# Performance work log

Measured on AMD Instinct MI355X. Metric: run time of the kernel, lower is better.

Reference implementation:

```python
import jax, jax.numpy as jnp
import numpy as np
from jax import lax

C = 256  # in_channels == out_channels
DN = ('NCHW', 'OIHW', 'NCHW')


def _haar_kernels(Cc, dtype):
    # Faithfully reproduce the torch buffer construction, INCLUDING its layout:
    # filters has shape (4*C, 1, 2, 2) with filters[f*C + c] = base[f]; the grouped
    # conv (groups=C) then applies filters[oc] (= base[oc // C]) to input channel oc // 4.
    lo = np.array([0.5, 0.5], np.float32)
    hi = np.array([0.5, -0.5], np.float32)
    # torch: dec_a.unsqueeze(0)*dec_b.unsqueeze(1) -> [i,j] = a[j]*b[i] = outer(b, a)
    dec_base = np.stack([np.outer(lo, lo), np.outer(hi, lo), np.outer(lo, hi), np.outer(hi, hi)], 0)
    dec_k = dec_base[np.arange(4 * Cc) // Cc][:, None]  # (4C, 1, 2, 2)
    rlo = np.array([1.0, 1.0], np.float32)
    rhi = np.array([1.0, -1.0], np.float32)
    rec_base = np.stack([np.outer(rlo, rlo), np.outer(rhi, rlo), np.outer(rlo, rhi), np.outer(rhi, rhi)], 0) / 2.0
    # conv_transpose2d(stride=2, groups=C) weight (4C, 1, 2, 2) with w[f*C + c] = rec_base[f].
    # Equivalent regular grouped conv (feature_group_count=C) kernel (C, 4, 2, 2):
    # K[g, f] = flip2(w[4g + f, 0]), applied with lhs_dilation=2, padding=1.
    w = rec_base[np.arange(4 * Cc) // Cc]
    rec_k = w.reshape(Cc, 4, 2, 2)[:, :, ::-1, ::-1].copy()
    return jnp.asarray(dec_k, dtype), jnp.asarray(rec_k, dtype)


def _dw(x, w, b=None):
    # depthwise 3x3 conv, padding=1
    y = lax.conv_general_dilated(x, w, (1, 1), [(1, 1), (1, 1)],
                                 feature_group_count=x.shape[1], dimension_numbers=DN)
    return y if b is None else y + b[None, :, None, None]


def setup_inputs() -> dict:
    key = jax.random.key(0)
    ks = jax.random.split(key, 12)
    p = lambda k, s: jax.random.normal(k, s, jnp.float32) * 0.1
    return {
        'x': jax.random.normal(ks[0], (4, C, 224, 224), jnp.float32),
        'base_w': p(ks[1], (C, 1, 3, 3)),
        'base_b': p(ks[2], (C,)),
        'base_scale': jnp.ones((1, C, 1, 1), jnp.float32),
        'wavelet_scale': jnp.full((1, C, 1, 1), 0.1, jnp.float32),
        'w_ll': p(ks[3], (C, 1, 3, 3)),
        'w_lh0': p(ks[4], (C, 1, 3, 3)),
        'w_hl0': p(ks[5], (C, 1, 3, 3)),
        'w_hh0': p(ks[6], (C, 1, 3, 3)),
        'w_lh1': p(ks[7], (C, 1, 3, 3)),
        'w_hl1': p(ks[8], (C, 1, 3, 3)),
        'w_hh1': p(ks[9], (C, 1, 3, 3)),
    }


def reference(x, base_w, base_b, base_scale, wavelet_scale, w_ll,
              w_lh0, w_hl0, w_hh0, w_lh1, w_hl1, w_hh1):
    B, Cc, H, W = x.shape
    dec_k, rec_k = _haar_kernels(Cc, x.dtype)

    def decompose(z):
        y = lax.conv_general_dilated(z, dec_k, (2, 2), 'VALID',
                                     feature_group_count=Cc, dimension_numbers=DN)
        y = y.reshape(B, Cc, 4, y.shape[-2], y.shape[-1])
        return y[:, :, 0], y[:, :, 1], y[:, :, 2], y[:, :, 3]  # ll, lh, hl, hh

    def reconstruct(ll, lh, hl, hh):
        comb = jnp.stack([ll, lh, hl, hh], 2).reshape(B, Cc * 4, ll.shape[-2], ll.shape[-1])
        return lax.conv_general_dilated(comb, rec_k, (1, 1), [(1, 1), (1, 1)],
                                        lhs_dilation=(2, 2), feature_group_count=Cc,
                                        dimension_numbers=DN)

    divisor = 4  # 2 ** depth
    pad_h, pad_w = (-H) % divisor, (-W) % divisor
    xp = jnp.pad(x, ((0, 0), (0, 0), (0, pad_h), (0, pad_w)), mode='reflect') if (pad_h or pad_w) else x

    # recursive DWT (depth=2)
    ll0, lh0, hl0, hh0 = decompose(xp)
    ll1, lh1, hl1, hh1 = decompose(ll0)

    # per-subband depthwise convs, then recursive IDWT
    x_wt = _dw(ll1, w_ll)  # only the deepest level's LL conv is used
    x_wt = reconstruct(x_wt, _dw(lh1, w_lh1), _dw(hl1, w_hl1), _dw(hh1, w_hh1))
    x_wt = reconstruct(x_wt, _dw(lh0, w_lh0), _dw(hl0, w_hl0), _dw(hh0, w_hh0))
    x_wt = x_wt[:, :, :H, :W] * wavelet_scale

    x_base = _dw(x, base_w, base_b) * base_scale
    return x_base + x_wt
```

## Files before the change

kernel.cpp:

```cpp
#include <hip/hip_runtime.h>


#define HH 224
#define WW 224
#define CC 256
#define BB 4
#define XS_S 68
#define T0_S 36

__global__ __launch_bounds__(256) void wtconv_fused(
    const float* __restrict__ x,
    const float* __restrict__ base_w,
    const float* __restrict__ base_b,
    const float* __restrict__ base_scale,
    const float* __restrict__ wavelet_scale,
    const float* __restrict__ w_ll,
    const float* __restrict__ w_lh0,
    const float* __restrict__ w_hl0,
    const float* __restrict__ w_hh0,
    const float* __restrict__ w_lh1,
    const float* __restrict__ w_hl1,
    const float* __restrict__ w_hh1,
    float* __restrict__ out)
{
    __shared__ float xs[64][XS_S];
    __shared__ float t0s[32][T0_S];
    __shared__ float t1s[16][18];
    __shared__ float a1s[14][14];
    __shared__ float a0s[28][28];

    const int tid  = threadIdx.x;
    const int bid  = blockIdx.x;
    const int tile = bid & 15;
    const int c    = (bid >> 4) & 255;
    const int b    = bid >> 12;
    const int tj   = tile & 3;
    const int ti   = tile >> 2;
    const int R0   = ti * 56;
    const int C0   = tj * 56;

    const int f = c >> 6;
    const float sR = (f & 1) ? -1.f : 1.f;
    const float sC = (f & 2) ? -1.f : 1.f;

    float ws1[9], ws0[9], bw[9];
#pragma unroll
    for (int j = 0; j < 9; ++j) {
        const int o = c * 9 + j;
        ws1[j] = w_ll[o] + w_lh1[o] + w_hl1[o] + w_hh1[o];
        ws0[j] = w_lh0[o] + w_hl0[o] + w_hh0[o];
        bw[j]  = base_w[o];
    }
    const float bb  = base_b[c];
    const float bsc = base_scale[c];
    const float wsc = wavelet_scale[c];

    const float* xp = x   + (size_t)(b * CC + c) * (HH * WW);
    float*       op = out + (size_t)(b * CC + c) * (HH * WW);

    {
        const int k  = tid & 15;
        const int rp = tid >> 4;
        const int gc = C0 - 4 + 4 * k;
        const bool cok = (gc >= 0) & (gc < WW);
        float4 v0 = make_float4(0.f, 0.f, 0.f, 0.f);
#pragma unroll
        for (int it = 0; it < 4; ++it) {
            const int row = 2 * rp + (it & 1) + 32 * (it >> 1);
            const int gr  = R0 - 4 + row;
            float4 v = make_float4(0.f, 0.f, 0.f, 0.f);
            if (cok && gr >= 0 && gr < HH)
                v = *(const float4*)(xp + gr * WW + gc);
            *(float4*)&xs[row][4 * k] = v;
            if (it & 1) {
                const float e = (v0.x + sC * v0.y) + sR * (v.x + sC * v.y);
                const float o = (v0.z + sC * v0.w) + sR * (v.z + sC * v.w);
                const int t0r = rp + 16 * (it >> 1);
                *(float2*)&t0s[t0r][2 * k] = make_float2(0.25f * e, 0.25f * o);
            } else {
                v0 = v;
            }
        }
    }
    __syncthreads();

    if (tid < 64) {
        const int m = tid >> 2;
        const int n = 4 * (tid & 3);
        const float4 A  = *(const float4*)&t0s[2 * m][2 * n];
        const float4 Bq = *(const float4*)&t0s[2 * m][2 * n + 4];
        const float4 Cq = *(const float4*)&t0s[2 * m + 1][2 * n];
        const float4 Dq = *(const float4*)&t0s[2 * m + 1][2 * n + 4];
        const float v0v = 0.25f * ((A.x + sC * A.y) + sR * (Cq.x + sC * Cq.y));
        const float v1v = 0.25f * ((A.z + sC * A.w) + sR * (Cq.z + sC * Cq.w));
        const float v2v = 0.25f * ((Bq.x + sC * Bq.y) + sR * (Dq.x + sC * Dq.y));
        const float v3v = 0.25f * ((Bq.z + sC * Bq.w) + sR * (Dq.z + sC * Dq.w));
        *(float2*)&t1s[m][n]     = make_float2(v0v, v1v);
        *(float2*)&t1s[m][n + 2] = make_float2(v2v, v3v);
    }
    __syncthreads();

    if (tid < 98) {
        const int k = tid / 7;
        const int l = 2 * (tid % 7);
        float acc0 = 0.f, acc1 = 0.f;
#pragma unroll
        for (int u = 0; u < 3; ++u) {
            const float2 p = *(const float2*)&t1s[k + u][l];
            const float2 q = *(const float2*)&t1s[k + u][l + 2];
            acc0 += p.x * ws1[3 * u] + p.y * ws1[3 * u + 1] + q.x * ws1[3 * u + 2];
            acc1 += p.y * ws1[3 * u] + q.x * ws1[3 * u + 1] + q.y * ws1[3 * u + 2];
        }
        *(float2*)&a1s[k][l] = make_float2(acc0, acc1);
    }
    __syncthreads();

    if (tid < 196) {
        const int i  = tid / 7;
        const int j7 = tid % 7;
        const int j  = 4 * j7;
        float a0 = 0.f, a1v = 0.f, a2 = 0.f, a3 = 0.f;
#pragma unroll
        for (int u = 0; u < 3; ++u) {
            const float4 A  = *(const float4*)&t0s[i + 1 + u][j];
            const float4 Bq = *(const float4*)&t0s[i + 1 + u][j + 4];
            const float c1 = A.y, c2 = A.z, c3 = A.w, c4 = Bq.x, c5 = Bq.y, c6 = Bq.z;
            const float w0 = ws0[3 * u], w1 = ws0[3 * u + 1], w2 = ws0[3 * u + 2];
            a0  += c1 * w0 + c2 * w1 + c3 * w2;
            a1v += c2 * w0 + c3 * w1 + c4 * w2;
            a2  += c3 * w0 + c4 * w1 + c5 * w2;
            a3  += c4 * w0 + c5 * w1 + c6 * w2;
        }
        const float2 ap = *(const float2*)&a1s[i >> 1][2 * j7];
        const float e = 0.5f * ((i & 1) ? sR : 1.f);
        const float o = e * sC;
        float4 r;
        r.x = a0  + e * ap.x;
        r.y = a1v + o * ap.x;
        r.z = a2  + e * ap.y;
        r.w = a3  + o * ap.y;
        *(float4*)&a0s[i][j] = r;
    }
    __syncthreads();

    if (tid < 196) {
        const int cg   = tid % 14;
        const int band = tid / 14;
        const int r0   = 4 * band;
        const int xc   = 4 * cg + 3;
        float h[6][6];
#pragma unroll
        for (int rr = 0; rr < 6; ++rr) {
            const float* row = &xs[r0 + 3 + rr][0];
            const float  s0v = row[xc];
            const float4 q   = *(const float4*)&row[xc + 1];
            const float  s1v = row[xc + 5];
            h[rr][0] = s0v; h[rr][1] = q.x; h[rr][2] = q.y;
            h[rr][3] = q.z; h[rr][4] = q.w; h[rr][5] = s1v;
        }
        const float we = wsc * 0.5f;
#pragma unroll
        for (int rr = 0; rr < 4; ++rr) {
            const int r = r0 + rr;
            float acc[4];
#pragma unroll
            for (int t = 0; t < 4; ++t) {
                acc[t] = h[rr][t]     * bw[0] + h[rr][t + 1]     * bw[1] + h[rr][t + 2]     * bw[2]
                       + h[rr + 1][t] * bw[3] + h[rr + 1][t + 1] * bw[4] + h[rr + 1][t + 2] * bw[5]
                       + h[rr + 2][t] * bw[6] + h[rr + 2][t + 1] * bw[7] + h[rr + 2][t + 2] * bw[8];
            }
            const float2 ap = *(const float2*)&a0s[r >> 1][2 * cg];
            const float w0 = (r & 1) ? we * sR : we;
            const float w1 = w0 * sC;
            float4 o;
            o.x = (acc[0] + bb) * bsc + w0 * ap.x;
            o.y = (acc[1] + bb) * bsc + w1 * ap.x;
            o.z = (acc[2] + bb) * bsc + w0 * ap.y;
            o.w = (acc[3] + bb) * bsc + w1 * ap.y;
            *(float4*)(op + (size_t)(R0 + r) * WW + C0 + 4 * cg) = o;
        }
    }
}

extern "C" void kernel_launch(void* const* d_in, const int* in_sizes, int n_in,
                              void* d_out, int out_size, void* d_ws, size_t ws_size,
                              hipStream_t stream) {
    const float* x             = (const float*)d_in[0];
    const float* base_w        = (const float*)d_in[1];
    const float* base_b        = (const float*)d_in[2];
    const float* base_scale    = (const float*)d_in[3];
    const float* wavelet_scale = (const float*)d_in[4];
    const float* w_ll          = (const float*)d_in[5];
    const float* w_lh0         = (const float*)d_in[6];
    const float* w_hl0         = (const float*)d_in[7];
    const float* w_hh0         = (const float*)d_in[8];
    const float* w_lh1         = (const float*)d_in[9];
    const float* w_hl1         = (const float*)d_in[10];
    const float* w_hh1         = (const float*)d_in[11];
    float* out                 = (float*)d_out;

    dim3 grid(BB * CC * 16);
    dim3 block(256);
    hipLaunchKernelGGL(wtconv_fused, grid, block, 0, stream,
                       x, base_w, base_b, base_scale, wavelet_scale,
                       w_ll, w_lh0, w_hl0, w_hh0, w_lh1, w_hl1, w_hh1, out);
}
```

Baseline: 390.4 us.

## Process two adjacent tiles per block with register prefetch of second tile

Each block now handles two horizontally adjacent 56x56 tiles of the same channel instead of one, halving the grid. Global loads for both tiles are issued up front into registers, so the second tile's memory latency overlaps the first tile's compute. Per-channel weight setup is paid once per two tiles, and __launch_bounds__ adds a min-blocks hint of 4. The risk is higher register pressure from holding 32 extra floats, plus fewer blocks in flight.

```diff
diff --git a/kernel.cpp b/kernel.cpp
--- a/kernel.cpp
+++ b/kernel.cpp
@@ -8,7 +8,7 @@
 #define XS_S 68
 #define T0_S 36
 
-__global__ __launch_bounds__(256) void wtconv_fused(
+__global__ __launch_bounds__(256, 4) void wtconv_fused(
     const float* __restrict__ x,
     const float* __restrict__ base_w,
     const float* __restrict__ base_b,
@@ -31,13 +31,14 @@
 
     const int tid  = threadIdx.x;
     const int bid  = blockIdx.x;
-    const int tile = bid & 15;
-    const int c    = (bid >> 4) & 255;
-    const int b    = bid >> 12;
-    const int tj   = tile & 3;
-    const int ti   = tile >> 2;
+    const int pr   = bid & 7;
+    const int c    = (bid >> 3) & 255;
+    const int b    = bid >> 11;
+    const int tA   = 2 * pr;
+    const int ti   = tA >> 2;
     const int R0   = ti * 56;
-    const int C0   = tj * 56;
+    const int C0A  = (tA & 3) * 56;
+    const int C0B  = C0A + 56;
 
     const int f = c >> 6;
     const float sR = (f & 1) ? -1.f : 1.f;
@@ -58,128 +59,162 @@
     const float* xp = x   + (size_t)(b * CC + c) * (HH * WW);
     float*       op = out + (size_t)(b * CC + c) * (HH * WW);
 
+    const int k  = tid & 15;
+    const int rp = tid >> 4;
+    float4 vA[4], vB[4];
     {
-        const int k  = tid & 15;
-        const int rp = tid >> 4;
-        const int gc = C0 - 4 + 4 * k;
-        const bool cok = (gc >= 0) & (gc < WW);
-        float4 v0 = make_float4(0.f, 0.f, 0.f, 0.f);
+        const int gcA = C0A - 4 + 4 * k;
+        const int gcB = C0B - 4 + 4 * k;
+        const bool cokA = (gcA >= 0) & (gcA < WW);
+        const bool cokB = (gcB < WW);
+#pragma unroll
+        for (int it = 0; it < 4; ++it) {
+            const int gr  = R0 - 4 + 2 * rp + (it & 1) + 32 * (it >> 1);
+            const bool rok = (gr >= 0) & (gr < HH);
+            float4 a = make_float4(0.f, 0.f, 0.f, 0.f);
+            float4 bq = make_float4(0.f, 0.f, 0.f, 0.f);
+            if (rok & cokA) a  = *(const float4*)(xp + gr * WW + gcA);
+            if (rok & cokB) bq = *(const float4*)(xp + gr * WW + gcB);
+            vA[it] = a; vB[it] = bq;
+        }
+    }
+
+    auto t0_store = [&](const float4* v) {
+#pragma unroll
+        for (int h = 0; h < 2; ++h) {
+            const float4 v0 = v[2 * h];
+            const float4 v1 = v[2 * h + 1];
+            const float e = (v0.x + sC * v0.y) + sR * (v1.x + sC * v1.y);
+            const float o = (v0.z + sC * v0.w) + sR * (v1.z + sC * v1.w);
+            *(float2*)&t0s[rp + 16 * h][2 * k] = make_float2(0.25f * e, 0.25f * o);
+        }
+    };
+    auto xs_store = [&](const float4* v) {
 #pragma unroll
         for (int it = 0; it < 4; ++it) {
             const int row = 2 * rp + (it & 1) + 32 * (it >> 1);
-            const int gr  = R0 - 4 + row;
-            float4 v = make_float4(0.f, 0.f, 0.f, 0.f);
-            if (cok && gr >= 0 && gr < HH)
-                v = *(const float4*)(xp + gr * WW + gc);
-            *(float4*)&xs[row][4 * k] = v;
-            if (it & 1) {
-                const float e = (v0.x + sC * v0.y) + sR * (v.x + sC * v.y);
-                const float o = (v0.z + sC * v0.w) + sR * (v.z + sC * v.w);
-                const int t0r = rp + 16 * (it >> 1);
-                *(float2*)&t0s[t0r][2 * k] = make_float2(0.25f * e, 0.25f * o);
-            } else {
-                v0 = v;
-            }
-        }
-    }
-    __syncthreads();
-
-    if (tid < 64) {
-        const int m = tid >> 2;
-        const int n = 4 * (tid & 3);
-        const float4 A  = *(const float4*)&t0s[2 * m][2 * n];
-        const float4 Bq = *(const float4*)&t0s[2 * m][2 * n + 4];
-        const float4 Cq = *(const float4*)&t0s[2 * m + 1][2 * n];
-        const float4 Dq = *(const float4*)&t0s[2 * m + 1][2 * n + 4];
-        const float v0v = 0.25f * ((A.x + sC * A.y) + sR * (Cq.x + sC * Cq.y));
-        const float v1v = 0.25f * ((A.z + sC * A.w) + sR * (Cq.z + sC * Cq.w));
-        const float v2v = 0.25f * ((Bq.x + sC * Bq.y) + sR * (Dq.x + sC * Dq.y));
-        const float v3v = 0.25f * ((Bq.z + sC * Bq.w) + sR * (Dq.z + sC * Dq.w));
-        *(float2*)&t1s[m][n]     = make_float2(v0v, v1v);
-        *(float2*)&t1s[m][n + 2] = make_float2(v2v, v3v);
-    }
-    __syncthreads();
-
-    if (tid < 98) {
-        const int k = tid / 7;
-        const int l = 2 * (tid % 7);
-        float acc0 = 0.f, acc1 = 0.f;
-#pragma unroll
-        for (int u = 0; u < 3; ++u) {
-            const float2 p = *(const float2*)&t1s[k + u][l];
-            const float2 q = *(const float2*)&t1s[k + u][l + 2];
-            acc0 += p.x * ws1[3 * u] + p.y * ws1[3 * u + 1] + q.x * ws1[3 * u + 2];
-            acc1 += p.y * ws1[3 * u] + q.x * ws1[3 * u + 1] + q.y * ws1[3 * u + 2];
-        }
-        *(float2*)&a1s[k][l] = make_float2(acc0, acc1);
-    }
-    __syncthreads();
-
-    if (tid < 196) {
-        const int i  = tid / 7;
-        const int j7 = tid % 7;
-        const int j  = 4 * j7;
-        float a0 = 0.f, a1v = 0.f, a2 = 0.f, a3 = 0.f;
-#pragma unroll
-        for (int u = 0; u < 3; ++u) {
-            const float4 A  = *(const float4*)&t0s[i + 1 + u][j];
-            const float4 Bq = *(const float4*)&t0s[i + 1 + u][j + 4];
-            const float c1 = A.y, c2 = A.z, c3 = A.w, c4 = Bq.x, c5 = Bq.y, c6 = Bq.z;
-            const float w0 = ws0[3 * u], w1 = ws0[3 * u + 1], w2 = ws0[3 * u + 2];
-            a0  += c1 * w0 + c2 * w1 + c3 * w2;
-            a1v += c2 * w0 + c3 * w1 + c4 * w2;
-            a2  += c3 * w0 + c4 * w1 + c5 * w2;
-            a3  += c4 * w0 + c5 * w1 + c6 * w2;
-        }
-        const float2 ap = *(const float2*)&a1s[i >> 1][2 * j7];
-        const float e = 0.5f * ((i & 1) ? sR : 1.f);
-        const float o = e * sC;
-        float4 r;
-        r.x = a0  + e * ap.x;
-        r.y = a1v + o * ap.x;
-        r.z = a2  + e * ap.y;
-        r.w = a3  + o * ap.y;
-        *(float4*)&a0s[i][j] = r;
-    }
-    __syncthreads();
-
-    if (tid < 196) {
-        const int cg   = tid % 14;
-        const int band = tid / 14;
-        const int r0   = 4 * band;
-        const int xc   = 4 * cg + 3;
-        float h[6][6];
-#pragma unroll
-        for (int rr = 0; rr < 6; ++rr) {
-            const float* row = &xs[r0 + 3 + rr][0];
-            const float  s0v = row[xc];
-            const float4 q   = *(const float4*)&row[xc + 1];
-            const float  s1v = row[xc + 5];
-            h[rr][0] = s0v; h[rr][1] = q.x; h[rr][2] = q.y;
-            h[rr][3] = q.z; h[rr][4] = q.w; h[rr][5] = s1v;
-        }
-        const float we = wsc * 0.5f;
-#pragma unroll
-        for (int rr = 0; rr < 4; ++rr) {
-            const int r = r0 + rr;
-            float acc[4];
-#pragma unroll
-            for (int t = 0; t < 4; ++t) {
-                acc[t] = h[rr][t]     * bw[0] + h[rr][t + 1]     * bw[1] + h[rr][t + 2]     * bw[2]
-                       + h[rr + 1][t] * bw[3] + h[rr + 1][t + 1] * bw[4] + h[rr + 1][t + 2] * bw[5]
-                       + h[rr + 2][t] * bw[6] + h[rr + 2][t + 1] * bw[7] + h[rr + 2][t + 2] * bw[8];
-            }
-            const float2 ap = *(const float2*)&a0s[r >> 1][2 * cg];
-            const float w0 = (r & 1) ? we * sR : we;
-            const float w1 = w0 * sC;
-            float4 o;
-            o.x = (acc[0] + bb) * bsc + w0 * ap.x;
-            o.y = (acc[1] + bb) * bsc + w1 * ap.x;
-            o.z = (acc[2] + bb) * bsc + w0 * ap.y;
-            o.w = (acc[3] + bb) * bsc + w1 * ap.y;
-            *(float4*)(op + (size_t)(R0 + r) * WW + C0 + 4 * cg) = o;
-        }
-    }
+            *(float4*)&xs[row][4 * k] = v[it];
+        }
+    };
+    auto t1_phase = [&]() {
+        if (tid < 64) {
+            const int m = tid >> 2;
+            const int n = 4 * (tid & 3);
+            const float4 A  = *(const float4*)&t0s[2 * m][2 * n];
+            const float4 Bq = *(const float4*)&t0s[2 * m][2 * n + 4];
+            const float4 Cq = *(const float4*)&t0s[2 * m + 1][2 * n];
+            const float4 Dq = *(const float4*)&t0s[2 * m + 1][2 * n + 4];
+            const float v0v = 0.25f * ((A.x + sC * A.y) + sR * (Cq.x + sC * Cq.y));
+            const float v1v = 0.25f * ((A.z + sC * A.w) + sR * (Cq.z + sC * Cq.w));
+            const float v2v = 0.25f * ((Bq.x + sC * Bq.y) + sR * (Dq.x + sC * Dq.y));
+            const float v3v = 0.25f * ((Bq.z + sC * Bq.w) + sR * (Dq.z + sC * Dq.w));
+            *(float2*)&t1s[m][n]     = make_float2(v0v, v1v);
+            *(float2*)&t1s[m][n + 2] = make_float2(v2v, v3v);
+        }
+    };
+    auto a1_phase = [&]() {
+        if (tid < 98) {
+            const int kk = tid / 7;
+            const int l  = 2 * (tid % 7);
+            float acc0 = 0.f, acc1 = 0.f;
+#pragma unroll
+            for (int u = 0; u < 3; ++u) {
+                const float2 p = *(const float2*)&t1s[kk + u][l];
+                const float2 q = *(const float2*)&t1s[kk + u][l + 2];
+                acc0 += p.x * ws1[3 * u] + p.y * ws1[3 * u + 1] + q.x * ws1[3 * u + 2];
+                acc1 += p.y * ws1[3 * u] + q.x * ws1[3 * u + 1] + q.y * ws1[3 * u + 2];
+            }
+            *(float2*)&a1s[kk][l] = make_float2(acc0, acc1);
+        }
+    };
+    auto a0_phase = [&]() {
+        if (tid < 196) {
+            const int i  = tid / 7;
+            const int j7 = tid % 7;
+            const int j  = 4 * j7;
+            float a0 = 0.f, a1v = 0.f, a2 = 0.f, a3 = 0.f;
+#pragma unroll
+            for (int u = 0; u < 3; ++u) {
+                const float4 A  = *(const float4*)&t0s[i + 1 + u][j];
+                const float4 Bq = *(const float4*)&t0s[i + 1 + u][j + 4];
+                const float c1 = A.y, c2 = A.z, c3 = A.w, c4 = Bq.x, c5 = Bq.y, c6 = Bq.z;
+                const float w0 = ws0[3 * u], w1 = ws0[3 * u + 1], w2 = ws0[3 * u + 2];
+                a0  += c1 * w0 + c2 * w1 + c3 * w2;
+                a1v += c2 * w0 + c3 * w1 + c4 * w2;
+                a2  += c3 * w0 + c4 * w1 + c5 * w2;
+                a3  += c4 * w0 + c5 * w1 + c6 * w2;
+            }
+            const float2 ap = *(const float2*)&a1s[i >> 1][2 * j7];
+            const float e = 0.5f * ((i & 1) ? sR : 1.f);
+            const float o = e * sC;
+            float4 r;
+            r.x = a0  + e * ap.x;
+            r.y = a1v + o * ap.x;
+            r.z = a2  + e * ap.y;
+            r.w = a3  + o * ap.y;
+            *(float4*)&a0s[i][j] = r;
+        }
+    };
+    auto phase6 = [&](int C0) {
+        if (tid < 196) {
+            const int cg   = tid % 14;
+            const int band = tid / 14;
+            const int r0   = 4 * band;
+            const int xc   = 4 * cg + 3;
+            float h[6][6];
+#pragma unroll
+            for (int rr = 0; rr < 6; ++rr) {
+                const float* row = &xs[r0 + 3 + rr][0];
+                const float  s0v = row[xc];
+                const float4 q   = *(const float4*)&row[xc + 1];
+                const float  s1v = row[xc + 5];
+                h[rr][0] = s0v; h[rr][1] = q.x; h[rr][2] = q.y;
+                h[rr][3] = q.z; h[rr][4] = q.w; h[rr][5] = s1v;
+            }
+            const float we = wsc * 0.5f;
+#pragma unroll
+            for (int rr = 0; rr < 4; ++rr) {
+                const int r = r0 + rr;
+                float acc[4];
+#pragma unroll
+                for (int t = 0; t < 4; ++t) {
+                    acc[t] = h[rr][t]     * bw[0] + h[rr][t + 1]     * bw[1] + h[rr][t + 2]     * bw[2]
+                           + h[rr + 1][t] * bw[3] + h[rr + 1][t + 1] * bw[4] + h[rr + 1][t + 2] * bw[5]
+                           + h[rr + 2][t] * bw[6] + h[rr + 2][t + 1] * bw[7] + h[rr + 2][t + 2] * bw[8];
+                }
+                const float2 ap = *(const float2*)&a0s[r >> 1][2 * cg];
+                const float w0 = (r & 1) ? we * sR : we;
+                const float w1 = w0 * sC;
+                float4 o;
+                o.x = (acc[0] + bb) * bsc + w0 * ap.x;
+                o.y = (acc[1] + bb) * bsc + w1 * ap.x;
+                o.z = (acc[2] + bb) * bsc + w0 * ap.y;
+                o.w = (acc[3] + bb) * bsc + w1 * ap.y;
+                *(float4*)(op + (size_t)(R0 + r) * WW + C0 + 4 * cg) = o;
+            }
+        }
+    };
+
+    xs_store(vA);
+    t0_store(vA);
+    __syncthreads();
+    t1_phase();
+    __syncthreads();
+    a1_phase();
+    __syncthreads();
+    a0_phase();
+    __syncthreads();
+    phase6(C0A);
+    t0_store(vB);
+    __syncthreads();
+    xs_store(vB);
+    t1_phase();
+    __syncthreads();
+    a1_phase();
+    __syncthreads();
+    a0_phase();
+    __syncthreads();
+    phase6(C0B);
 }
 
 extern "C" void kernel_launch(void* const* d_in, const int* in_sizes, int n_in,
@@ -199,7 +234,7 @@
     const float* w_hh1         = (const float*)d_in[11];
     float* out                 = (float*)d_out;
 
-    dim3 grid(BB * CC * 16);
+    dim3 grid(BB * CC * 8);
     dim3 block(256);
     hipLaunchKernelGGL(wtconv_fused, grid, block, 0, stream,
                        x, base_w, base_b, base_scale, wavelet_scale,
```

Result: faster. 376.6 us (-3.5%).

## Give each wavefront its own tile and replace block barriers with register shuffles

Applied to the files above, without the earlier changes.

Each 64-lane wavefront now owns an independent 32x56 tile with its own shared-memory slices, so the block-wide __syncthreads barriers become per-wave lgkmcnt waits. The input tile is held in registers, and the base 3x3 depthwise conv gets its neighbours through cross-lane shuffles in a rolling-row window instead of a staged shared-memory copy. Uniform weights are pushed to scalar registers with readfirstlane, and the grid becomes 7x256x4 with a launch_bounds occupancy hint. In exchange, some lanes are wasted on halo columns and rows, and register pressure rises from the ten held float4 rows.

```diff
diff --git a/kernel.cpp b/kernel.cpp
--- a/kernel.cpp
+++ b/kernel.cpp
@@ -5,10 +5,14 @@
 #define WW 224
 #define CC 256
 #define BB 4
-#define XS_S 68
-#define T0_S 36
-
-__global__ __launch_bounds__(256) void wtconv_fused(
+
+#define WAVE_SYNC asm volatile("s_waitcnt lgkmcnt(0)" ::: "memory")
+
+__device__ __forceinline__ float rfl(float v) {
+    return __uint_as_float(__builtin_amdgcn_readfirstlane(__float_as_uint(v)));
+}
+
+__global__ __launch_bounds__(256, 6) void wtconv_fused(
     const float* __restrict__ x,
     const float* __restrict__ base_w,
     const float* __restrict__ base_b,
@@ -23,21 +27,22 @@
     const float* __restrict__ w_hh1,
     float* __restrict__ out)
 {
-    __shared__ float xs[64][XS_S];
-    __shared__ float t0s[32][T0_S];
-    __shared__ float t1s[16][18];
-    __shared__ float a1s[14][14];
-    __shared__ float a0s[28][28];
-
-    const int tid  = threadIdx.x;
-    const int bid  = blockIdx.x;
-    const int tile = bid & 15;
-    const int c    = (bid >> 4) & 255;
-    const int b    = bid >> 12;
-    const int tj   = tile & 3;
-    const int ti   = tile >> 2;
-    const int R0   = ti * 56;
-    const int C0   = tj * 56;
+    __shared__ float t0s[4][20][34];
+    __shared__ float t1s[4][10][17];
+    __shared__ float a1s[4][8][15];
+    __shared__ float a0s[4][16][30];
+
+    const int tid   = threadIdx.x;
+    const int wid   = tid >> 6;
+    const int lane  = tid & 63;
+    const int k     = lane & 15;
+    const int rp    = lane >> 4;
+    const int strip = blockIdx.x;
+    const int c     = blockIdx.y;
+    const int b     = blockIdx.z;
+
+    const int R0 = 32 * strip;
+    const int C0 = 56 * wid;
 
     const int f = c >> 6;
     const float sR = (f & 1) ? -1.f : 1.f;
@@ -47,138 +52,145 @@
 #pragma unroll
     for (int j = 0; j < 9; ++j) {
         const int o = c * 9 + j;
-        ws1[j] = w_ll[o] + w_lh1[o] + w_hl1[o] + w_hh1[o];
-        ws0[j] = w_lh0[o] + w_hl0[o] + w_hh0[o];
-        bw[j]  = base_w[o];
-    }
-    const float bb  = base_b[c];
-    const float bsc = base_scale[c];
-    const float wsc = wavelet_scale[c];
+        ws1[j] = rfl(w_ll[o] + w_lh1[o] + w_hl1[o] + w_hh1[o]);
+        ws0[j] = rfl(w_lh0[o] + w_hl0[o] + w_hh0[o]);
+        bw[j]  = rfl(base_w[o]);
+    }
+    const float bb  = rfl(base_b[c]);
+    const float bsc = rfl(base_scale[c]);
+    const float wsc = rfl(wavelet_scale[c]);
 
     const float* xp = x   + (size_t)(b * CC + c) * (HH * WW);
     float*       op = out + (size_t)(b * CC + c) * (HH * WW);
 
+    float4 X[10];
     {
-        const int k  = tid & 15;
-        const int rp = tid >> 4;
         const int gc = C0 - 4 + 4 * k;
-        const bool cok = (gc >= 0) & (gc < WW);
-        float4 v0 = make_float4(0.f, 0.f, 0.f, 0.f);
-#pragma unroll
-        for (int it = 0; it < 4; ++it) {
-            const int row = 2 * rp + (it & 1) + 32 * (it >> 1);
-            const int gr  = R0 - 4 + row;
+        const bool cok = (gc >= 0) & (gc <= WW - 4);
+#pragma unroll
+        for (int i = 0; i < 10; ++i) {
+            const int gr = R0 - 4 + 10 * rp + i;
             float4 v = make_float4(0.f, 0.f, 0.f, 0.f);
-            if (cok && gr >= 0 && gr < HH)
-                v = *(const float4*)(xp + gr * WW + gc);
-            *(float4*)&xs[row][4 * k] = v;
-            if (it & 1) {
-                const float e = (v0.x + sC * v0.y) + sR * (v.x + sC * v.y);
-                const float o = (v0.z + sC * v0.w) + sR * (v.z + sC * v.w);
-                const int t0r = rp + 16 * (it >> 1);
-                *(float2*)&t0s[t0r][2 * k] = make_float2(0.25f * e, 0.25f * o);
-            } else {
-                v0 = v;
+            if (cok & (gr >= 0) & (gr < HH))
+                v = *(const float4*)(xp + (size_t)gr * WW + gc);
+            X[i] = v;
+        }
+    }
+
+#pragma unroll
+    for (int a = 0; a < 5; ++a) {
+        const float4 v0 = X[2 * a];
+        const float4 v1 = X[2 * a + 1];
+        const float e = (v0.x + sC * v0.y) + sR * (v1.x + sC * v1.y);
+        const float o = (v0.z + sC * v0.w) + sR * (v1.z + sC * v1.w);
+        *(float2*)&t0s[wid][5 * rp + a][2 * k] = make_float2(0.25f * e, 0.25f * o);
+    }
+    WAVE_SYNC;
+
+#pragma unroll
+    for (int j = 0; j < 3; ++j) {
+        const int e = lane + 64 * j;
+        if (e < 160) {
+            const int m = e >> 4;
+            const int n = e & 15;
+            const float2 p = *(const float2*)&t0s[wid][2 * m][2 * n];
+            const float2 q = *(const float2*)&t0s[wid][2 * m + 1][2 * n];
+            t1s[wid][m][n] = 0.25f * ((p.x + sC * p.y) + sR * (q.x + sC * q.y));
+        }
+    }
+    WAVE_SYNC;
+
+    const int col  = lane & 15;
+    const int row4 = lane >> 4;
+    if (col < 14) {
+#pragma unroll
+        for (int j = 0; j < 2; ++j) {
+            const int g = row4 + 4 * j;
+            float acc = 0.f;
+#pragma unroll
+            for (int u = 0; u < 3; ++u) {
+                acc += t1s[wid][g + u][col]     * ws1[3 * u]
+                     + t1s[wid][g + u][col + 1] * ws1[3 * u + 1]
+                     + t1s[wid][g + u][col + 2] * ws1[3 * u + 2];
             }
-        }
-    }
-    __syncthreads();
-
-    if (tid < 64) {
-        const int m = tid >> 2;
-        const int n = 4 * (tid & 3);
-        const float4 A  = *(const float4*)&t0s[2 * m][2 * n];
-        const float4 Bq = *(const float4*)&t0s[2 * m][2 * n + 4];
-        const float4 Cq = *(const float4*)&t0s[2 * m + 1][2 * n];
-        const float4 Dq = *(const float4*)&t0s[2 * m + 1][2 * n + 4];
-        const float v0v = 0.25f * ((A.x + sC * A.y) + sR * (Cq.x + sC * Cq.y));
-        const float v1v = 0.25f * ((A.z + sC * A.w) + sR * (Cq.z + sC * Cq.w));
-        const float v2v = 0.25f * ((Bq.x + sC * Bq.y) + sR * (Dq.x + sC * Dq.y));
-        const float v3v = 0.25f * ((Bq.z + sC * Bq.w) + sR * (Dq.z + sC * Dq.w));
-        *(float2*)&t1s[m][n]     = make_float2(v0v, v1v);
-        *(float2*)&t1s[m][n + 2] = make_float2(v2v, v3v);
-    }
-    __syncthreads();
-
-    if (tid < 98) {
-        const int k = tid / 7;
-        const int l = 2 * (tid % 7);
-        float acc0 = 0.f, acc1 = 0.f;
-#pragma unroll
-        for (int u = 0; u < 3; ++u) {
-            const float2 p = *(const float2*)&t1s[k + u][l];
-            const float2 q = *(const float2*)&t1s[k + u][l + 2];
-            acc0 += p.x * ws1[3 * u] + p.y * ws1[3 * u + 1] + q.x * ws1[3 * u + 2];
-            acc1 += p.y * ws1[3 * u] + q.x * ws1[3 * u + 1] + q.y * ws1[3 * u + 2];
-        }
-        *(float2*)&a1s[k][l] = make_float2(acc0, acc1);
-    }
-    __syncthreads();
-
-    if (tid < 196) {
-        const int i  = tid / 7;
-        const int j7 = tid % 7;
-        const int j  = 4 * j7;
-        float a0 = 0.f, a1v = 0.f, a2 = 0.f, a3 = 0.f;
-#pragma unroll
-        for (int u = 0; u < 3; ++u) {
-            const float4 A  = *(const float4*)&t0s[i + 1 + u][j];
-            const float4 Bq = *(const float4*)&t0s[i + 1 + u][j + 4];
-            const float c1 = A.y, c2 = A.z, c3 = A.w, c4 = Bq.x, c5 = Bq.y, c6 = Bq.z;
-            const float w0 = ws0[3 * u], w1 = ws0[3 * u + 1], w2 = ws0[3 * u + 2];
-            a0  += c1 * w0 + c2 * w1 + c3 * w2;
-            a1v += c2 * w0 + c3 * w1 + c4 * w2;
-            a2  += c3 * w0 + c4 * w1 + c5 * w2;
-            a3  += c4 * w0 + c5 * w1 + c6 * w2;
-        }
-        const float2 ap = *(const float2*)&a1s[i >> 1][2 * j7];
-        const float e = 0.5f * ((i & 1) ? sR : 1.f);
-        const float o = e * sC;
-        float4 r;
-        r.x = a0  + e * ap.x;
-        r.y = a1v + o * ap.x;
-        r.z = a2  + e * ap.y;
-        r.w = a3  + o * ap.y;
-        *(float4*)&a0s[i][j] = r;
-    }
-    __syncthreads();
-
-    if (tid < 196) {
-        const int cg   = tid % 14;
-        const int band = tid / 14;
-        const int r0   = 4 * band;
-        const int xc   = 4 * cg + 3;
-        float h[6][6];
-#pragma unroll
-        for (int rr = 0; rr < 6; ++rr) {
-            const float* row = &xs[r0 + 3 + rr][0];
-            const float  s0v = row[xc];
-            const float4 q   = *(const float4*)&row[xc + 1];
-            const float  s1v = row[xc + 5];
-            h[rr][0] = s0v; h[rr][1] = q.x; h[rr][2] = q.y;
-            h[rr][3] = q.z; h[rr][4] = q.w; h[rr][5] = s1v;
-        }
-        const float we = wsc * 0.5f;
-#pragma unroll
-        for (int rr = 0; rr < 4; ++rr) {
-            const int r = r0 + rr;
-            float acc[4];
-#pragma unroll
-            for (int t = 0; t < 4; ++t) {
-                acc[t] = h[rr][t]     * bw[0] + h[rr][t + 1]     * bw[1] + h[rr][t + 2]     * bw[2]
-                       + h[rr + 1][t] * bw[3] + h[rr + 1][t + 1] * bw[4] + h[rr + 1][t + 2] * bw[5]
-                       + h[rr + 2][t] * bw[6] + h[rr + 2][t + 1] * bw[7] + h[rr + 2][t + 2] * bw[8];
+            a1s[wid][g][col] = acc;
+        }
+    }
+    WAVE_SYNC;
+
+    if (col < 14) {
+#pragma unroll
+        for (int j = 0; j < 4; ++j) {
+            const int r = row4 + 4 * j;
+            float s0 = 0.f, s1 = 0.f;
+#pragma unroll
+            for (int u = 0; u < 3; ++u) {
+                const float2 A  = *(const float2*)&t0s[wid][r + 1 + u][2 * col];
+                const float2 Bq = *(const float2*)&t0s[wid][r + 1 + u][2 * col + 2];
+                const float2 Cq = *(const float2*)&t0s[wid][r + 1 + u][2 * col + 4];
+                const float w0 = ws0[3 * u], w1 = ws0[3 * u + 1], w2 = ws0[3 * u + 2];
+                s0 += A.y  * w0 + Bq.x * w1 + Bq.y * w2;
+                s1 += Bq.x * w0 + Bq.y * w1 + Cq.x * w2;
             }
-            const float2 ap = *(const float2*)&a0s[r >> 1][2 * cg];
-            const float w0 = (r & 1) ? we * sR : we;
-            const float w1 = w0 * sC;
-            float4 o;
-            o.x = (acc[0] + bb) * bsc + w0 * ap.x;
-            o.y = (acc[1] + bb) * bsc + w1 * ap.x;
-            o.z = (acc[2] + bb) * bsc + w0 * ap.y;
-            o.w = (acc[3] + bb) * bsc + w1 * ap.y;
-            *(float4*)(op + (size_t)(R0 + r) * WW + C0 + 4 * cg) = o;
-        }
+            const float av = a1s[wid][r >> 1][col];
+            const float e = 0.5f * ((r & 1) ? sR : 1.f);
+            const float o = e * sC;
+            *(float2*)&a0s[wid][r][2 * col] = make_float2(s0 + e * av, s1 + o * av);
+        }
+    }
+    WAVE_SYNC;
+
+    const int kk  = k - 1;
+    const bool kok = (k >= 1) & (k <= 14);
+    const int kc  = kok ? kk : 0;
+    const float we = wsc * 0.5f;
+
+    float4 w0v, w1v;
+    {
+        const float4 t8 = X[8], t9 = X[9];
+        w0v.x = __shfl(t8.x, lane - 16); w0v.y = __shfl(t8.y, lane - 16);
+        w0v.z = __shfl(t8.z, lane - 16); w0v.w = __shfl(t8.w, lane - 16);
+        w1v.x = __shfl(t9.x, lane - 16); w1v.y = __shfl(t9.y, lane - 16);
+        w1v.z = __shfl(t9.z, lane - 16); w1v.w = __shfl(t9.w, lane - 16);
+    }
+    float l0 = __shfl(w0v.w, lane - 1), r0 = __shfl(w0v.x, lane + 1);
+    float l1 = __shfl(w1v.w, lane - 1), r1 = __shfl(w1v.x, lane + 1);
+
+#pragma unroll
+    for (int jj = 0; jj < 10; ++jj) {
+        const float4 w2v = X[jj];
+        const float l2 = __shfl(w2v.w, lane - 1);
+        const float r2 = __shfl(w2v.x, lane + 1);
+        const int o = 10 * rp - 5 + jj;
+
+        const float acc0 = l0    * bw[0] + w0v.x * bw[1] + w0v.y * bw[2]
+                         + l1    * bw[3] + w1v.x * bw[4] + w1v.y * bw[5]
+                         + l2    * bw[6] + w2v.x * bw[7] + w2v.y * bw[8];
+        const float acc1 = w0v.x * bw[0] + w0v.y * bw[1] + w0v.z * bw[2]
+                         + w1v.x * bw[3] + w1v.y * bw[4] + w1v.z * bw[5]
+                         + w2v.x * bw[6] + w2v.y * bw[7] + w2v.z * bw[8];
+        const float acc2 = w0v.y * bw[0] + w0v.z * bw[1] + w0v.w * bw[2]
+                         + w1v.y * bw[3] + w1v.z * bw[4] + w1v.w * bw[5]
+                         + w2v.y * bw[6] + w2v.z * bw[7] + w2v.w * bw[8];
+        const float acc3 = w0v.z * bw[0] + w0v.w * bw[1] + r0    * bw[2]
+                         + w1v.z * bw[3] + w1v.w * bw[4] + r1    * bw[5]
+                         + w2v.z * bw[6] + w2v.w * bw[7] + r2    * bw[8];
+
+        const int oc = o < 0 ? 0 : (o > 31 ? 31 : o);
+        const float2 ap = *(const float2*)&a0s[wid][oc >> 1][2 * kc];
+        const float ww0 = (o & 1) ? we * sR : we;
+        const float ww1 = ww0 * sC;
+
+        if (kok & (o >= 0) & (o <= 31)) {
+            float4 ov;
+            ov.x = (acc0 + bb) * bsc + ww0 * ap.x;
+            ov.y = (acc1 + bb) * bsc + ww1 * ap.x;
+            ov.z = (acc2 + bb) * bsc + ww0 * ap.y;
+            ov.w = (acc3 + bb) * bsc + ww1 * ap.y;
+            *(float4*)(op + (size_t)(R0 + o) * WW + C0 + 4 * kk) = ov;
+        }
+        w0v = w1v; l0 = l1; r0 = r1;
+        w1v = w2v; l1 = l2; r1 = r2;
     }
 }
 
@@ -199,7 +211,7 @@
     const float* w_hh1         = (const float*)d_in[11];
     float* out                 = (float*)d_out;
 
-    dim3 grid(BB * CC * 16);
+    dim3 grid(7, CC, BB);
     dim3 block(256);
     hipLaunchKernelGGL(wtconv_fused, grid, block, 0, stream,
                        x, base_w, base_b, base_scale, wavelet_scale,
```

Result: no change. 387.1 us (-0.8%).
